# Kernel tuning notes

Measured on AMD Instinct MI355X. Metric: run time of the kernel, lower is better.

Reference implementation:

```python
import jax, jax.numpy as jnp
import numpy as np


def setup_inputs() -> dict:
    key = jax.random.key(0)
    X = jax.random.normal(key, (8192, 64, 64), dtype=jnp.float32)
    return {"X": X}


def reference(X):
    # ensure_sym: symmetrize
    S = 0.5 * (X + jnp.swapaxes(X, -1, -2))  # [B, n, n]
    # matrix exp via eigendecomposition: S = V diag(w) V^T -> exp(S) = V diag(exp(w)) V^T
    w, V = jnp.linalg.eigh(S)                # w: [B, n], V: [B, n, n]
    out = jnp.einsum('bik,bk,bjk->bij', V, jnp.exp(w), V)
    return out
```

## Files before the change

### kernel.cpp

```cpp
#include <hip/hip_runtime.h>


typedef _Float16 half2v __attribute__((ext_vector_type(2)));
typedef _Float16 half4v __attribute__((ext_vector_type(4)));
typedef _Float16 half8v __attribute__((ext_vector_type(8)));
typedef float f32x4 __attribute__((ext_vector_type(4)));

constexpr int N = 64;

__device__ __forceinline__ void split2(float v0, float v1, half2v& h, half2v& l) {
    h = __builtin_bit_cast(half2v, __builtin_amdgcn_cvt_pkrtz(v0, v1));
    l = __builtin_bit_cast(half2v, __builtin_amdgcn_cvt_pkrtz((v0 - (float)h[0]) * 2048.0f,
                                                              (v1 - (float)h[1]) * 2048.0f));
}

__device__ __forceinline__ void split4(float v0, float v1, float v2, float v3,
                                       half4v& h, half4v& l) {
    half2v h01, l01, h23, l23;
    split2(v0, v1, h01, l01);
    split2(v2, v3, h23, l23);
    h[0] = h01[0]; h[1] = h01[1]; h[2] = h23[0]; h[3] = h23[1];
    l[0] = l01[0]; l[1] = l01[1]; l[2] = l23[0]; l[3] = l23[1];
}

__device__ __forceinline__ int swz(int row, int colbyte) {
    return (row * 128 + colbyte) ^ ((row & 7) << 4);
}

__device__ __forceinline__ half8v frag16(const char* p, int tile, int ks, int lane) {
    const int row = tile * 16 + (lane & 15);
    const int cb = (ks * 32 + ((lane >> 4) << 3)) * 2;
    return *reinterpret_cast<const half8v*>(p + swz(row, cb));
}

__device__ __forceinline__ f32x4 mm_split(const half8v* ah, const half8v* al,
                                          const half8v* bh, const half8v* bl) {
    f32x4 c = {0.f, 0.f, 0.f, 0.f};
    c = __builtin_amdgcn_mfma_f32_16x16x32_f16(al[0], bh[0], c, 0, 0, 0);
    c = __builtin_amdgcn_mfma_f32_16x16x32_f16(al[1], bh[1], c, 0, 0, 0);
    c = __builtin_amdgcn_mfma_f32_16x16x32_f16(ah[0], bl[0], c, 0, 0, 0);
    c = __builtin_amdgcn_mfma_f32_16x16x32_f16(ah[1], bl[1], c, 0, 0, 0);
    #pragma unroll
    for (int e = 0; e < 4; ++e) c[e] *= (1.0f / 2048.0f);
    c = __builtin_amdgcn_mfma_f32_16x16x32_f16(ah[0], bh[0], c, 0, 0, 0);
    c = __builtin_amdgcn_mfma_f32_16x16x32_f16(ah[1], bh[1], c, 0, 0, 0);
    return c;
}

__global__ __launch_bounds__(256, 3) void expm64_kernel(const float* __restrict__ X,
                                                        float* __restrict__ out) {
    __shared__ alignas(16) char lds[49152];
    char* Th = lds;
    char* Tl = lds + 8192;
    char* Ph = lds + 16384;
    char* Pl = lds + 24576;
    char* Qh = lds + 32768;
    char* Ql = lds + 40960;
    float* Xs = reinterpret_cast<float*>(lds + 16384);

    const int t = threadIdx.x;
    const int lane = t & 63;
    const int wv = t >> 6;
    const int wr = (wv >> 1) << 1;
    const int wc = (wv & 1) << 1;
    const size_t base = (size_t)blockIdx.x * (N * N);

    {
        const float4* src = reinterpret_cast<const float4*>(X + base);
        float4* dst = reinterpret_cast<float4*>(Xs);
        #pragma unroll
        for (int i = 0; i < 4; ++i) dst[t + 256 * i] = src[t + 256 * i];
    }
    __syncthreads();

    const int r0 = (t >> 4) << 2;
    const int c0 = (t & 15) << 2;

    float tv[4][4];
    #pragma unroll
    for (int i = 0; i < 4; ++i) {
        #pragma unroll
        for (int j = 0; j < 4; ++j)
            tv[i][j] = (Xs[(r0 + i) * 64 + (c0 + j)] + Xs[(c0 + j) * 64 + (r0 + i)]) * (1.0f / 32.0f);
        half4v h, l;
        split4(tv[i][0], tv[i][1], tv[i][2], tv[i][3], h, l);
        *reinterpret_cast<half4v*>(Th + swz(r0 + i, c0 * 2)) = h;
        *reinterpret_cast<half4v*>(Tl + swz(r0 + i, c0 * 2)) = l;
    }
    __syncthreads();

    {
        const float c10 = 2.755731922398589e-07f;
        const float c11 = 2.505210838544172e-08f;
        #pragma unroll
        for (int i = 0; i < 4; ++i) {
            float v[4];
            #pragma unroll
            for (int j = 0; j < 4; ++j)
                v[j] = c11 * tv[i][j] + ((r0 + i == c0 + j) ? c10 : 0.0f);
            half4v h, l;
            split4(v[0], v[1], v[2], v[3], h, l);
            *reinterpret_cast<half4v*>(Ph + swz(r0 + i, c0 * 2)) = h;
            *reinterpret_cast<half4v*>(Pl + swz(r0 + i, c0 * 2)) = l;
        }
    }
    __syncthreads();

    {
        half8v ah[2][2], al[2][2], bh[2][2], bl[2][2];
        #pragma unroll
        for (int a = 0; a < 2; ++a)
            #pragma unroll
            for (int ks = 0; ks < 2; ++ks) {
                ah[a][ks] = frag16(Th, wr + a, ks, lane);
                al[a][ks] = frag16(Tl, wr + a, ks, lane);
                bh[a][ks] = frag16(Th, wc + a, ks, lane);
                bl[a][ks] = frag16(Tl, wc + a, ks, lane);
            }
        #pragma unroll
        for (int a = 0; a < 2; ++a)
            #pragma unroll
            for (int b = 0; b < 2; ++b) {
                f32x4 acc = mm_split(ah[a], al[a], bh[b], bl[b]);
                const int rowp = (wc + b) * 16 + (lane & 15);
                const int colp = (wr + a) * 16 + ((lane >> 4) << 2);
                half4v h, l;
                split4(acc[0], acc[1], acc[2], acc[3], h, l);
                *reinterpret_cast<half4v*>(Qh + swz(rowp, colp * 2)) = h;
                *reinterpret_cast<half4v*>(Ql + swz(rowp, colp * 2)) = l;
            }
    }
    __syncthreads();

    {
        const float ce[5] = { 2.48015873015873e-05f, 1.388888888888889e-03f,
                              4.1666666666666664e-02f, 0.5f, 1.0f };
        const float co[5] = { 2.7557319223985893e-06f, 1.984126984126984e-04f,
                              8.333333333333333e-03f, 1.6666666666666666e-01f, 1.0f };
        half8v t2h[2][2], t2l[2][2];
        #pragma unroll
        for (int b = 0; b < 2; ++b)
            #pragma unroll
            for (int ks = 0; ks < 2; ++ks) {
                t2h[b][ks] = frag16(Qh, wc + b, ks, lane);
                t2l[b][ks] = frag16(Ql, wc + b, ks, lane);
            }
        #pragma unroll
        for (int s = 0; s < 5; ++s) {
            half8v ah[2][2], al[2][2];
            #pragma unroll
            for (int a = 0; a < 2; ++a)
                #pragma unroll
                for (int ks = 0; ks < 2; ++ks) {
                    ah[a][ks] = frag16(Ph, wr + a, ks, lane);
                    al[a][ks] = frag16(Pl, wr + a, ks, lane);
                }
            f32x4 acc[2][2];
            #pragma unroll
            for (int a = 0; a < 2; ++a)
                #pragma unroll
                for (int b = 0; b < 2; ++b)
                    acc[a][b] = mm_split(ah[a], al[a], t2h[b], t2l[b]);
            __syncthreads();
            const float fin = (s == 4) ? 0.5f : 1.0f;
            #pragma unroll
            for (int a = 0; a < 2; ++a)
                #pragma unroll
                for (int b = 0; b < 2; ++b) {
                    const int rowp = (wc + b) * 16 + (lane & 15);
                    const int colp = (wr + a) * 16 + ((lane >> 4) << 2);
                    const half4v th = *reinterpret_cast<const half4v*>(Th + swz(rowp, colp * 2));
                    const half4v tl = *reinterpret_cast<const half4v*>(Tl + swz(rowp, colp * 2));
                    float v[4];
                    #pragma unroll
                    for (int e = 0; e < 4; ++e) {
                        const int grow = colp + e;
                        const int gcol = rowp;
                        const float tval = (float)th[e] + (float)tl[e] * (1.0f / 2048.0f);
                        v[e] = (acc[a][b][e] + co[s] * tval
                                + ((grow == gcol) ? ce[s] : 0.0f)) * fin;
                    }
                    half4v h, l;
                    split4(v[0], v[1], v[2], v[3], h, l);
                    *reinterpret_cast<half4v*>(Ph + swz(rowp, colp * 2)) = h;
                    *reinterpret_cast<half4v*>(Pl + swz(rowp, colp * 2)) = l;
                }
            __syncthreads();
        }
    }

    #pragma unroll
    for (int s = 0; s < 4; ++s) {
        half8v ah[2][2], al[2][2], bh[2][2], bl[2][2];
        #pragma unroll
        for (int a = 0; a < 2; ++a)
            #pragma unroll
            for (int ks = 0; ks < 2; ++ks) {
                ah[a][ks] = frag16(Ph, wr + a, ks, lane);
                al[a][ks] = frag16(Pl, wr + a, ks, lane);
                bh[a][ks] = frag16(Ph, wc + a, ks, lane);
                bl[a][ks] = frag16(Pl, wc + a, ks, lane);
            }
        f32x4 acc[2][2];
        #pragma unroll
        for (int a = 0; a < 2; ++a)
            #pragma unroll
            for (int b = 0; b < 2; ++b)
                acc[a][b] = mm_split(ah[a], al[a], bh[b], bl[b]);
        if (s < 3) {
            __syncthreads();
            #pragma unroll
            for (int a = 0; a < 2; ++a)
                #pragma unroll
                for (int b = 0; b < 2; ++b) {
                    const int rowp = (wc + b) * 16 + (lane & 15);
                    const int colp = (wr + a) * 16 + ((lane >> 4) << 2);
                    half4v h, l;
                    split4(acc[a][b][0], acc[a][b][1], acc[a][b][2], acc[a][b][3], h, l);
                    *reinterpret_cast<half4v*>(Ph + swz(rowp, colp * 2)) = h;
                    *reinterpret_cast<half4v*>(Pl + swz(rowp, colp * 2)) = l;
                }
            __syncthreads();
        } else {
            float* o = out + base;
            #pragma unroll
            for (int a = 0; a < 2; ++a)
                #pragma unroll
                for (int b = 0; b < 2; ++b) {
                    const int row0 = (wr + a) * 16 + ((lane >> 4) << 2);
                    const int col  = (wc + b) * 16 + (lane & 15);
                    #pragma unroll
                    for (int e = 0; e < 4; ++e)
                        o[(row0 + e) * 64 + col] = acc[a][b][e] * 65536.0f;
                }
        }
    }
}

extern "C" void kernel_launch(void* const* d_in, const int* in_sizes, int n_in,
                              void* d_out, int out_size, void* d_ws, size_t ws_size,
                              hipStream_t stream) {
    const float* X = (const float*)d_in[0];
    float* out = (float*)d_out;
    const int batch = in_sizes[0] / (N * N);
    expm64_kernel<<<dim3(batch), dim3(256), 0, stream>>>(X, out);
}
```

Before: 313.2 us.

## Split each matrix across eight waves with 512-thread blocks

Doubles the threads per matrix from 256 to 512 so each wave computes a 16x32 output strip instead of a 32x32 block, and restructures the symmetrize/prep stage to 8 elements per thread. The goal is more resident waves per CU to hide LDS and MFMA latency, with lower register use per thread. In exchange, fragment reuse drops: A fragments are loaded per wave for fewer outputs and the T^2 operand is reloaded from LDS each polynomial step.

New measurement: 314.2 us. About the same (+0.3%).

```diff
diff --git a/kernel.cpp b/kernel.cpp
--- a/kernel.cpp
+++ b/kernel.cpp
@@ -14,13 +14,23 @@
                                                               (v1 - (float)h[1]) * 2048.0f));
 }
 
-__device__ __forceinline__ void split4(float v0, float v1, float v2, float v3,
-                                       half4v& h, half4v& l) {
+__device__ __forceinline__ void split4(const float* v, half4v& h, half4v& l) {
     half2v h01, l01, h23, l23;
-    split2(v0, v1, h01, l01);
-    split2(v2, v3, h23, l23);
+    split2(v[0], v[1], h01, l01);
+    split2(v[2], v[3], h23, l23);
     h[0] = h01[0]; h[1] = h01[1]; h[2] = h23[0]; h[3] = h23[1];
     l[0] = l01[0]; l[1] = l01[1]; l[2] = l23[0]; l[3] = l23[1];
+}
+
+__device__ __forceinline__ void split8(const float* v, half8v& h, half8v& l) {
+    half2v hh[4], ll[4];
+    #pragma unroll
+    for (int q = 0; q < 4; ++q) split2(v[2 * q], v[2 * q + 1], hh[q], ll[q]);
+    #pragma unroll
+    for (int q = 0; q < 4; ++q) {
+        h[2 * q] = hh[q][0]; h[2 * q + 1] = hh[q][1];
+        l[2 * q] = ll[q][0]; l[2 * q + 1] = ll[q][1];
+    }
 }
 
 __device__ __forceinline__ int swz(int row, int colbyte) {
@@ -47,7 +57,7 @@
     return c;
 }
 
-__global__ __launch_bounds__(256, 3) void expm64_kernel(const float* __restrict__ X,
+__global__ __launch_bounds__(512, 6) void expm64_kernel(const float* __restrict__ X,
                                                         float* __restrict__ out) {
     __shared__ alignas(16) char lds[49152];
     char* Th = lds;
@@ -61,74 +71,72 @@
     const int t = threadIdx.x;
     const int lane = t & 63;
     const int wv = t >> 6;
-    const int wr = (wv >> 1) << 1;
-    const int wc = (wv & 1) << 1;
+    const int wr = wv >> 1;
+    const int wc0 = (wv & 1) << 1;
     const size_t base = (size_t)blockIdx.x * (N * N);
 
     {
         const float4* src = reinterpret_cast<const float4*>(X + base);
         float4* dst = reinterpret_cast<float4*>(Xs);
-        #pragma unroll
-        for (int i = 0; i < 4; ++i) dst[t + 256 * i] = src[t + 256 * i];
-    }
-    __syncthreads();
-
-    const int r0 = (t >> 4) << 2;
-    const int c0 = (t & 15) << 2;
-
-    float tv[4][4];
-    #pragma unroll
-    for (int i = 0; i < 4; ++i) {
-        #pragma unroll
-        for (int j = 0; j < 4; ++j)
-            tv[i][j] = (Xs[(r0 + i) * 64 + (c0 + j)] + Xs[(c0 + j) * 64 + (r0 + i)]) * (1.0f / 32.0f);
-        half4v h, l;
-        split4(tv[i][0], tv[i][1], tv[i][2], tv[i][3], h, l);
-        *reinterpret_cast<half4v*>(Th + swz(r0 + i, c0 * 2)) = h;
-        *reinterpret_cast<half4v*>(Tl + swz(r0 + i, c0 * 2)) = l;
+        dst[t] = src[t];
+        dst[t + 512] = src[t + 512];
+    }
+    __syncthreads();
+
+    const int r = t >> 3;
+    const int c0 = (t & 7) << 3;
+
+    float tv[8];
+    {
+        #pragma unroll
+        for (int j = 0; j < 8; ++j)
+            tv[j] = (Xs[r * 64 + c0 + j] + Xs[(c0 + j) * 64 + r]) * (1.0f / 32.0f);
+        half8v h, l;
+        split8(tv, h, l);
+        *reinterpret_cast<half8v*>(Th + swz(r, c0 * 2)) = h;
+        *reinterpret_cast<half8v*>(Tl + swz(r, c0 * 2)) = l;
     }
     __syncthreads();
 
     {
         const float c10 = 2.755731922398589e-07f;
         const float c11 = 2.505210838544172e-08f;
-        #pragma unroll
-        for (int i = 0; i < 4; ++i) {
-            float v[4];
-            #pragma unroll
-            for (int j = 0; j < 4; ++j)
-                v[j] = c11 * tv[i][j] + ((r0 + i == c0 + j) ? c10 : 0.0f);
+        float v[8];
+        #pragma unroll
+        for (int j = 0; j < 8; ++j)
+            v[j] = c11 * tv[j] + ((r == c0 + j) ? c10 : 0.0f);
+        half8v h, l;
+        split8(v, h, l);
+        *reinterpret_cast<half8v*>(Ph + swz(r, c0 * 2)) = h;
+        *reinterpret_cast<half8v*>(Pl + swz(r, c0 * 2)) = l;
+    }
+    __syncthreads();
+
+    {
+        half8v ah[2], al[2], bh[2][2], bl[2][2];
+        #pragma unroll
+        for (int ks = 0; ks < 2; ++ks) {
+            ah[ks] = frag16(Th, wr, ks, lane);
+            al[ks] = frag16(Tl, wr, ks, lane);
+        }
+        #pragma unroll
+        for (int cb = 0; cb < 2; ++cb)
+            #pragma unroll
+            for (int ks = 0; ks < 2; ++ks) {
+                bh[cb][ks] = frag16(Th, wc0 + cb, ks, lane);
+                bl[cb][ks] = frag16(Tl, wc0 + cb, ks, lane);
+            }
+        #pragma unroll
+        for (int cb = 0; cb < 2; ++cb) {
+            f32x4 acc = mm_split(ah, al, bh[cb], bl[cb]);
+            const int rowp = (wc0 + cb) * 16 + (lane & 15);
+            const int colp = wr * 16 + ((lane >> 4) << 2);
+            float v[4] = { acc[0], acc[1], acc[2], acc[3] };
             half4v h, l;
-            split4(v[0], v[1], v[2], v[3], h, l);
-            *reinterpret_cast<half4v*>(Ph + swz(r0 + i, c0 * 2)) = h;
-            *reinterpret_cast<half4v*>(Pl + swz(r0 + i, c0 * 2)) = l;
-        }
-    }
-    __syncthreads();
-
-    {
-        half8v ah[2][2], al[2][2], bh[2][2], bl[2][2];
-        #pragma unroll
-        for (int a = 0; a < 2; ++a)
-            #pragma unroll
-            for (int ks = 0; ks < 2; ++ks) {
-                ah[a][ks] = frag16(Th, wr + a, ks, lane);
-                al[a][ks] = frag16(Tl, wr + a, ks, lane);
-                bh[a][ks] = frag16(Th, wc + a, ks, lane);
-                bl[a][ks] = frag16(Tl, wc + a, ks, lane);
-            }
-        #pragma unroll
-        for (int a = 0; a < 2; ++a)
-            #pragma unroll
-            for (int b = 0; b < 2; ++b) {
-                f32x4 acc = mm_split(ah[a], al[a], bh[b], bl[b]);
-                const int rowp = (wc + b) * 16 + (lane & 15);
-                const int colp = (wr + a) * 16 + ((lane >> 4) << 2);
-                half4v h, l;
-                split4(acc[0], acc[1], acc[2], acc[3], h, l);
-                *reinterpret_cast<half4v*>(Qh + swz(rowp, colp * 2)) = h;
-                *reinterpret_cast<half4v*>(Ql + swz(rowp, colp * 2)) = l;
-            }
+            split4(v, h, l);
+            *reinterpret_cast<half4v*>(Qh + swz(rowp, colp * 2)) = h;
+            *reinterpret_cast<half4v*>(Ql + swz(rowp, colp * 2)) = l;
+        }
     }
     __syncthreads();
 
@@ -137,102 +145,93 @@
                               4.1666666666666664e-02f, 0.5f, 1.0f };
         const float co[5] = { 2.7557319223985893e-06f, 1.984126984126984e-04f,
                               8.333333333333333e-03f, 1.6666666666666666e-01f, 1.0f };
-        half8v t2h[2][2], t2l[2][2];
-        #pragma unroll
-        for (int b = 0; b < 2; ++b)
+        #pragma unroll
+        for (int s = 0; s < 5; ++s) {
+            half8v ah[2], al[2], bh[2][2], bl[2][2];
             #pragma unroll
             for (int ks = 0; ks < 2; ++ks) {
-                t2h[b][ks] = frag16(Qh, wc + b, ks, lane);
-                t2l[b][ks] = frag16(Ql, wc + b, ks, lane);
-            }
-        #pragma unroll
-        for (int s = 0; s < 5; ++s) {
-            half8v ah[2][2], al[2][2];
-            #pragma unroll
-            for (int a = 0; a < 2; ++a)
+                ah[ks] = frag16(Ph, wr, ks, lane);
+                al[ks] = frag16(Pl, wr, ks, lane);
+            }
+            #pragma unroll
+            for (int cb = 0; cb < 2; ++cb)
                 #pragma unroll
                 for (int ks = 0; ks < 2; ++ks) {
-                    ah[a][ks] = frag16(Ph, wr + a, ks, lane);
-                    al[a][ks] = frag16(Pl, wr + a, ks, lane);
+                    bh[cb][ks] = frag16(Qh, wc0 + cb, ks, lane);
+                    bl[cb][ks] = frag16(Ql, wc0 + cb, ks, lane);
                 }
-            f32x4 acc[2][2];
-            #pragma unroll
-            for (int a = 0; a < 2; ++a)
+            f32x4 acc[2];
+            #pragma unroll
+            for (int cb = 0; cb < 2; ++cb)
+                acc[cb] = mm_split(ah, al, bh[cb], bl[cb]);
+            __syncthreads();
+            const float fin = (s == 4) ? 0.5f : 1.0f;
+            #pragma unroll
+            for (int cb = 0; cb < 2; ++cb) {
+                const int rowp = (wc0 + cb) * 16 + (lane & 15);
+                const int colp = wr * 16 + ((lane >> 4) << 2);
+                const half4v th = *reinterpret_cast<const half4v*>(Th + swz(rowp, colp * 2));
+                const half4v tl = *reinterpret_cast<const half4v*>(Tl + swz(rowp, colp * 2));
+                float v[4];
                 #pragma unroll
-                for (int b = 0; b < 2; ++b)
-                    acc[a][b] = mm_split(ah[a], al[a], t2h[b], t2l[b]);
-            __syncthreads();
-            const float fin = (s == 4) ? 0.5f : 1.0f;
-            #pragma unroll
-            for (int a = 0; a < 2; ++a)
-                #pragma unroll
-                for (int b = 0; b < 2; ++b) {
-                    const int rowp = (wc + b) * 16 + (lane & 15);
-                    const int colp = (wr + a) * 16 + ((lane >> 4) << 2);
-                    const half4v th = *reinterpret_cast<const half4v*>(Th + swz(rowp, colp * 2));
-                    const half4v tl = *reinterpret_cast<const half4v*>(Tl + swz(rowp, colp * 2));
-                    float v[4];
-                    #pragma unroll
-                    for (int e = 0; e < 4; ++e) {
-                        const int grow = colp + e;
-                        const int gcol = rowp;
-                        const float tval = (float)th[e] + (float)tl[e] * (1.0f / 2048.0f);
-                        v[e] = (acc[a][b][e] + co[s] * tval
-                                + ((grow == gcol) ? ce[s] : 0.0f)) * fin;
-                    }
-                    half4v h, l;
-                    split4(v[0], v[1], v[2], v[3], h, l);
-                    *reinterpret_cast<half4v*>(Ph + swz(rowp, colp * 2)) = h;
-                    *reinterpret_cast<half4v*>(Pl + swz(rowp, colp * 2)) = l;
+                for (int e = 0; e < 4; ++e) {
+                    const int grow = colp + e;
+                    const int gcol = rowp;
+                    const float tval = (float)th[e] + (float)tl[e] * (1.0f / 2048.0f);
+                    v[e] = (acc[cb][e] + co[s] * tval
+                            + ((grow == gcol) ? ce[s] : 0.0f)) * fin;
                 }
+                half4v h, l;
+                split4(v, h, l);
+                *reinterpret_cast<half4v*>(Ph + swz(rowp, colp * 2)) = h;
+                *reinterpret_cast<half4v*>(Pl + swz(rowp, colp * 2)) = l;
+            }
             __syncthreads();
         }
     }
 
     #pragma unroll
     for (int s = 0; s < 4; ++s) {
-        half8v ah[2][2], al[2][2], bh[2][2], bl[2][2];
-        #pragma unroll
-        for (int a = 0; a < 2; ++a)
+        half8v ah[2], al[2], bh[2][2], bl[2][2];
+        #pragma unroll
+        for (int ks = 0; ks < 2; ++ks) {
+            ah[ks] = frag16(Ph, wr, ks, lane);
+            al[ks] = frag16(Pl, wr, ks, lane);
+        }
+        #pragma unroll
+        for (int cb = 0; cb < 2; ++cb)
             #pragma unroll
             for (int ks = 0; ks < 2; ++ks) {
-                ah[a][ks] = frag16(Ph, wr + a, ks, lane);
-                al[a][ks] = frag16(Pl, wr + a, ks, lane);
-                bh[a][ks] = frag16(Ph, wc + a, ks, lane);
-                bl[a][ks] = frag16(Pl, wc + a, ks, lane);
-            }
-        f32x4 acc[2][2];
-        #pragma unroll
-        for (int a = 0; a < 2; ++a)
-            #pragma unroll
-            for (int b = 0; b < 2; ++b)
-                acc[a][b] = mm_split(ah[a], al[a], bh[b], bl[b]);
+                bh[cb][ks] = frag16(Ph, wc0 + cb, ks, lane);
+                bl[cb][ks] = frag16(Pl, wc0 + cb, ks, lane);
+            }
+        f32x4 acc[2];
+        #pragma unroll
+        for (int cb = 0; cb < 2; ++cb)
+            acc[cb] = mm_split(ah, al, bh[cb], bl[cb]);
         if (s < 3) {
             __syncthreads();
             #pragma unroll
-            for (int a = 0; a < 2; ++a)
-                #pragma unroll
-                for (int b = 0; b < 2; ++b) {
-                    const int rowp = (wc + b) * 16 + (lane & 15);
-                    const int colp = (wr + a) * 16 + ((lane >> 4) << 2);
-                    half4v h, l;
-                    split4(acc[a][b][0], acc[a][b][1], acc[a][b][2], acc[a][b][3], h, l);
-                    *reinterpret_cast<half4v*>(Ph + swz(rowp, colp * 2)) = h;
-                    *reinterpret_cast<half4v*>(Pl + swz(rowp, colp * 2)) = l;
-                }
+            for (int cb = 0; cb < 2; ++cb) {
+                const int rowp = (wc0 + cb) * 16 + (lane & 15);
+                const int colp = wr * 16 + ((lane >> 4) << 2);
+                float v[4] = { acc[cb][0], acc[cb][1], acc[cb][2], acc[cb][3] };
+                half4v h, l;
+                split4(v, h, l);
+                *reinterpret_cast<half4v*>(Ph + swz(rowp, colp * 2)) = h;
+                *reinterpret_cast<half4v*>(Pl + swz(rowp, colp * 2)) = l;
+            }
             __syncthreads();
         } else {
             float* o = out + base;
             #pragma unroll
-            for (int a = 0; a < 2; ++a)
+            for (int cb = 0; cb < 2; ++cb) {
+                const int row0 = wr * 16 + ((lane >> 4) << 2);
+                const int col  = (wc0 + cb) * 16 + (lane & 15);
                 #pragma unroll
-                for (int b = 0; b < 2; ++b) {
-                    const int row0 = (wr + a) * 16 + ((lane >> 4) << 2);
-                    const int col  = (wc + b) * 16 + (lane & 15);
-                    #pragma unroll
-                    for (int e = 0; e < 4; ++e)
-                        o[(row0 + e) * 64 + col] = acc[a][b][e] * 65536.0f;
-                }
+                for (int e = 0; e < 4; ++e)
+                    o[(row0 + e) * 64 + col] = acc[cb][e] * 65536.0f;
+            }
         }
     }
 }
@@ -243,5 +242,5 @@
     const float* X = (const float*)d_in[0];
     float* out = (float*)d_out;
     const int batch = in_sizes[0] / (N * N);
-    expm64_kernel<<<dim3(batch), dim3(256), 0, stream>>>(X, out);
-}
+    expm64_kernel<<<dim3(batch), dim3(512), 0, stream>>>(X, out);
+}
```
